# Kernel tuning notes

Hardware: AMD Instinct MI355X
Metric: run time of the kernel (lower is better)

Reference implementation:

```python
import jax, jax.numpy as jnp
import numpy as np

B, T, LEAF, A = 128, 50, 4880, 64
INTERNAL = 728
ATTN = 128   # attn_dim_size (GRU input)
RNN = 128    # rnn_dim_size
G = 128      # g_dim_size (== RNN, required by broadcast in forward)
NC = 283     # num_class
VERY_NEG = -1e30


def setup_inputs() -> dict:
    key = jax.random.key(0)
    ks = jax.random.split(key, 16)
    s = 0.05
    inputs_x = jax.random.uniform(ks[0], (B, T, LEAF), jnp.float32)
    inputs_f = jax.random.randint(ks[1], (B, T, A), 0, INTERNAL + 1)  # 0 = padding
    mask_seqs = jnp.ones((B, T), jnp.float32)
    dag_emb = jax.random.normal(ks[2], (LEAF, ATTN), jnp.float32) * s
    embed_a = jax.random.normal(ks[3], (INTERNAL + 1, G), jnp.float32) * s
    embed_a = embed_a.at[0].set(0.0)  # padding row
    # 2-layer GRU params (torch layout: [3H, in], gates r,z,n)
    Wih0 = jax.random.normal(ks[4], (3 * RNN, ATTN), jnp.float32) * s
    Whh0 = jax.random.normal(ks[5], (3 * RNN, RNN), jnp.float32) * s
    bih0 = jax.random.normal(ks[6], (3 * RNN,), jnp.float32) * s
    bhh0 = jax.random.normal(ks[7], (3 * RNN,), jnp.float32) * s
    Wih1 = jax.random.normal(ks[8], (3 * RNN, RNN), jnp.float32) * s
    Whh1 = jax.random.normal(ks[9], (3 * RNN, RNN), jnp.float32) * s
    bih1 = jax.random.normal(ks[10], (3 * RNN,), jnp.float32) * s
    bhh1 = jax.random.normal(ks[11], (3 * RNN,), jnp.float32) * s
    fc_w = jax.random.normal(ks[12], (NC, 2 * RNN), jnp.float32) * s
    fc_b = jax.random.normal(ks[13], (NC,), jnp.float32) * s
    return dict(inputs_x=inputs_x, inputs_f=inputs_f, mask_seqs=mask_seqs,
                dag_emb=dag_emb, embed_a=embed_a,
                Wih0=Wih0, Whh0=Whh0, bih0=bih0, bhh0=bhh0,
                Wih1=Wih1, Whh1=Whh1, bih1=bih1, bhh1=bhh1,
                fc_w=fc_w, fc_b=fc_b)


def _gru_layer(x, Wih, Whh, bih, bhh):
    # x: [B, T, I] -> out [B, T, H]; h0 = zeros
    H = Whh.shape[1]
    xW = jnp.einsum('bti,gi->btg', x, Wih) + bih  # [B,T,3H], precompute input gates
    h0 = jnp.zeros((x.shape[0], H), x.dtype)

    def step(h, xw_t):  # xw_t: [B,3H]
        gh = h @ Whh.T + bhh
        xr, xz, xn = jnp.split(xw_t, 3, axis=-1)
        hr, hz, hn = jnp.split(gh, 3, axis=-1)
        r = jax.nn.sigmoid(xr + hr)
        z = jax.nn.sigmoid(xz + hz)
        n = jnp.tanh(xn + r * hn)
        h_new = (1.0 - z) * n + z * h
        return h_new, h_new

    _, ys = jax.lax.scan(step, h0, jnp.swapaxes(xW, 0, 1))  # scan over T
    return jnp.swapaxes(ys, 0, 1)


def reference(inputs_x, inputs_f, mask_seqs, dag_emb, embed_a,
              Wih0, Whh0, bih0, bhh0, Wih1, Whh1, bih1, bhh1, fc_w, fc_b):
    # x = tanh(inputs_x @ dag_emb): [B,T,ATTN]
    x = jnp.tanh(jnp.einsum('btl,la->bta', inputs_x, dag_emb))
    # 2-layer GRU (no dropout at inference)
    h1 = _gru_layer(x, Wih0, Whh0, bih0, bhh0)
    out = _gru_layer(h1, Wih1, Whh1, bih1, bhh1)  # [B,T,RNN]
    # gather ancestor embeddings: [B,T,A,G]
    l = embed_a[inputs_f]
    # masked dot-product attention over ancestors
    hl = jnp.einsum('bth,btah->bta', out, l)
    mask_ans = inputs_f > 0
    hl = hl + jnp.where(mask_ans, 0.0, VERY_NEG)
    weights = jax.nn.softmax(hl, axis=-1)  # [B,T,A]
    k = jnp.einsum('bta,btah->bth', weights, l)
    s = jnp.concatenate([out, k], axis=-1)  # [B,T,2*RNN]
    output = jax.nn.sigmoid(s @ fc_w.T + fc_b)
    return output * mask_seqs[:, :, None]
```

## Files before the change

kernel.cpp:

```cpp
#include <hip/hip_runtime.h>
#include <math.h>

#define B_DIM 128
#define T_DIM 50
#define LEAF  4880
#define A_DIM 64
#define ATTN  128
#define RNN   128
#define NC    283
#define M_TOT (B_DIM*T_DIM)
#define KSPLIT 10
#define NCH 153
#define WT_PLANE (NCH*512*8)

using short8 = __attribute__((ext_vector_type(8))) short;
using short4v = __attribute__((ext_vector_type(4))) short;
using f32x4  = __attribute__((ext_vector_type(4))) float;

__device__ __forceinline__ float sigmoidf_(float x) {
  return 1.0f / (1.0f + __expf(-x));
}
__device__ __forceinline__ float tanhf_fast(float x) {
  x = fminf(fmaxf(x, -15.f), 15.f);
  float e = __expf(2.f * x);
  return (e - 1.f) * __builtin_amdgcn_rcpf(e + 1.f);
}

__device__ __forceinline__ unsigned short f32_to_bf16_rne(float f) {
  unsigned int u = __float_as_uint(f);
  unsigned int r = u + 0x7FFFu + ((u >> 16) & 1u);
  return (unsigned short)(r >> 16);
}
__device__ __forceinline__ float bf16_bits_to_f32(unsigned short b) {
  return __uint_as_float(((unsigned int)b) << 16);
}

__global__ __launch_bounds__(256) void k_prep(
    const float* __restrict__ Wd,
    const float* __restrict__ Wih0, const float* __restrict__ Wih1,
    const float* __restrict__ fcw,
    unsigned short* __restrict__ Wt,
    unsigned short* __restrict__ Bt0, unsigned short* __restrict__ Bt1,
    unsigned short* __restrict__ Bt2) {
  const int bx = blockIdx.x;
  const int tid = threadIdx.x;
  if (bx < 306) {
    const int u = bx * 256 + tid;
    const int c = u >> 9, rem = u & 511;
    const int nt = rem >> 6, lane = rem & 63;
    const int n = nt * 16 + (lane & 15);
    const int kb = c * 32 + ((lane >> 4) << 3);
    short8 h8, l8;
    #pragma unroll
    for (int j = 0; j < 8; ++j) {
      int k = kb + j;
      float v = (k < LEAF) ? Wd[(size_t)k * 128 + n] : 0.0f;
      unsigned short hb = f32_to_bf16_rne(v);
      unsigned short lb = f32_to_bf16_rne(v - bf16_bits_to_f32(hb));
      h8[j] = (short)hb;
      l8[j] = (short)lb;
    }
    *(short8*)&Wt[(size_t)u * 8] = h8;
    *(short8*)&Wt[(size_t)WT_PLANE + (size_t)u * 8] = l8;
  } else {
    const float* src; unsigned short* dst; int N, K, s0;
    if (bx < 330)      { src = Wih0; dst = Bt0; N = 384; K = 128; s0 = (bx - 306) * 256; }
    else if (bx < 354) { src = Wih1; dst = Bt1; N = 384; K = 128; s0 = (bx - 330) * 256; }
    else               { src = fcw;  dst = Bt2; N = NC;  K = 256; s0 = (bx - 354) * 256; }
    const int s = s0 + tid;
    const int PL = (K / 32) * 24 * 512;
    const int kc = s / (24 * 64);
    const int r  = s % (24 * 64);
    const int nt = r >> 6, lane = r & 63;
    const int n  = nt * 16 + (lane & 15);
    const int kb = kc * 32 + ((lane >> 4) << 3);
    short8 h8, l8;
    #pragma unroll
    for (int j = 0; j < 8; ++j) {
      float v = (n < N) ? src[(size_t)n * K + kb + j] : 0.0f;
      unsigned short hb = f32_to_bf16_rne(v);
      unsigned short lb = f32_to_bf16_rne(v - bf16_bits_to_f32(hb));
      h8[j] = (short)hb;
      l8[j] = (short)lb;
    }
    *(short8*)&dst[(size_t)s * 8] = h8;
    *(short8*)&dst[(size_t)PL + (size_t)s * 8] = l8;
  }
}

__global__ __launch_bounds__(512, 8) void k_gemm_mfma(
    const float* __restrict__ Ax, const unsigned short* __restrict__ Wt,
    float* __restrict__ P) {
  __shared__ __align__(16) unsigned short As[2][4096];
  const int tid  = threadIdx.x;
  const int lane = tid & 63;
  const int w    = tid >> 6;
  const int M0   = blockIdx.x * 64;
  const int s    = blockIdx.y;
  const int c0   = (s * NCH) / KSPLIT;
  const int c1   = ((s + 1) * NCH) / KSPLIT;

  const int am = tid >> 3;
  const int kq = tid & 7;
  const float* pA = Ax + (size_t)(M0 + am) * LEAF;
  const int a_idx = (am >> 4) * 512 + ((am & 15) + 16 * (kq >> 1)) * 8 + (kq & 1) * 4;

  f32x4 acc[4];
  #pragma unroll
  for (int i = 0; i < 4; ++i) {
    #pragma unroll
    for (int q = 0; q < 4; ++q) acc[i][q] = 0.0f;
  }

  float4 rA_a, rA_b;
  short8 bh_a, bl_a, bh_b, bl_b;

  auto issueB = [&](int c, short8& bh, short8& bl) {
    const size_t o = ((size_t)c * 512 + w * 64 + lane) * 8;
    bh = *(const short8*)&Wt[o];
    bl = *(const short8*)&Wt[(size_t)WT_PLANE + o];
  };
  auto issueA = [&](int c, float4& ra) {
    int kk = c * 32 + kq * 4;
    kk = min(kk, LEAF - 4);
    ra = *(const float4*)(pA + kk);
  };
  auto storeA = [&](int p, float4 ra) {
    float v[4] = {ra.x, ra.y, ra.z, ra.w};
    short4v h4, l4;
    #pragma unroll
    for (int j = 0; j < 4; ++j) {
      unsigned short hb = f32_to_bf16_rne(v[j]);
      unsigned short lb = f32_to_bf16_rne(v[j] - bf16_bits_to_f32(hb));
      h4[j] = (short)hb;
      l4[j] = (short)lb;
    }
    *(short4v*)&As[p][a_idx] = h4;
    *(short4v*)&As[p][2048 + a_idx] = l4;
  };
  auto compute = [&](int p, const short8& bh, const short8& bl) {
    #pragma unroll
    for (int m = 0; m < 4; ++m) {
      short8 a_hi = *(const short8*)&As[p][m * 512 + lane * 8];
      short8 a_lo = *(const short8*)&As[p][2048 + m * 512 + lane * 8];
      acc[m] = __builtin_amdgcn_mfma_f32_16x16x32_bf16(a_hi, bl, acc[m], 0, 0, 0);
      acc[m] = __builtin_amdgcn_mfma_f32_16x16x32_bf16(a_lo, bh, acc[m], 0, 0, 0);
      acc[m] = __builtin_amdgcn_mfma_f32_16x16x32_bf16(a_hi, bh, acc[m], 0, 0, 0);
    }
  };

  {
    float4 ta;
    issueA(c0, ta);
    asm volatile("s_waitcnt vmcnt(0)" ::: "memory");
    storeA(0, ta);
    issueB(c0, bh_a, bl_a);
    asm volatile("" ::: "memory");
    if (c0 + 1 < c1) issueA(c0 + 1, rA_a);
    asm volatile("s_waitcnt lgkmcnt(0)" ::: "memory");
    __builtin_amdgcn_s_barrier();
    asm volatile("" ::: "memory");
  }

#define GEMM_ITER(BHc, BLc, BHn, BLn, RAc, RAn)                               \
  {                                                                           \
    const int p = (c - c0) & 1;                                               \
    const bool has1 = (c + 1 < c1), has2 = (c + 2 < c1);                      \
    if (has1) { issueB(c + 1, BHn, BLn); asm volatile("" ::: "memory"); }     \
    if (has2) { issueA(c + 2, RAn);      asm volatile("" ::: "memory"); }     \
    if (has1) {                                                               \
      if (has2) { asm volatile("s_waitcnt vmcnt(3)" ::: "memory"); }          \
      else      { asm volatile("s_waitcnt vmcnt(2)" ::: "memory"); }          \
    } else      { asm volatile("s_waitcnt vmcnt(0)" ::: "memory"); }          \
    compute(p, BHc, BLc);                                                     \
    if (has1) storeA(p ^ 1, RAc);                                             \
    asm volatile("s_waitcnt lgkmcnt(0)" ::: "memory");                        \
    __builtin_amdgcn_s_barrier();                                             \
    asm volatile("" ::: "memory");                                            \
    ++c;                                                                      \
  }

  int c = c0;
  while (c < c1) {
    GEMM_ITER(bh_a, bl_a, bh_b, bl_b, rA_a, rA_b);
    if (c < c1) GEMM_ITER(bh_b, bl_b, bh_a, bl_a, rA_b, rA_a);
  }
#undef GEMM_ITER

  float* outp = P + (size_t)s * ((size_t)M_TOT * 128);
  const int col0 = w * 16 + (lane & 15);
  #pragma unroll
  for (int m = 0; m < 4; ++m) {
    const int rbase = M0 + m * 16 + ((lane >> 4) << 2);
    #pragma unroll
    for (int r = 0; r < 4; ++r)
      outp[(size_t)(rbase + r) * 128 + col0] = acc[m][r];
  }
}

__global__ __launch_bounds__(256) void k_reduce_tanh(
    float* __restrict__ P, float* __restrict__ X) {
  const size_t i = ((size_t)blockIdx.x * 256 + threadIdx.x) * 4;
  float4 a = *(const float4*)&P[i];
  #pragma unroll
  for (int s = 1; s < KSPLIT; ++s) {
    float4 b = *(const float4*)&P[(size_t)s * (M_TOT * 128) + i];
    a.x += b.x; a.y += b.y; a.z += b.z; a.w += b.w;
  }
  a.x = tanhf(a.x); a.y = tanhf(a.y); a.z = tanhf(a.z); a.w = tanhf(a.w);
  *(float4*)&X[i] = a;
}

template<int KC, int ACT>
__global__ __launch_bounds__(512) void k_bn_mfma(
    const float* __restrict__ A, const unsigned short* __restrict__ Bt,
    const float* __restrict__ bias, const float* __restrict__ maskv,
    float* __restrict__ C, int N, int ldc) {
  constexpr int K  = KC * 32;
  constexpr int PL = KC * 24 * 512;
  __shared__ __align__(16) unsigned short As2[2][KC * 512];
  const int tid  = threadIdx.x;
  const int lane = tid & 63;
  const int w    = tid >> 6;
  const int mrow = blockIdx.x * 16;
  const int nt   = blockIdx.y * 8 + w;

  short8 bh[KC], bl[KC];
  #pragma unroll
  for (int kc = 0; kc < KC; ++kc) {
    const size_t o = ((size_t)(kc * 24 + nt) * 64 + lane) * 8;
    bh[kc] = *(const short8*)&Bt[o];
    bl[kc] = *(const short8*)&Bt[(size_t)PL + o];
  }

  const int am = tid >> 5;
  const int q0 = tid & 31;
  constexpr int NQ = K / 128;
  float4 av[NQ];
  #pragma unroll
  for (int i = 0; i < NQ; ++i)
    av[i] = *(const float4*)&A[(size_t)(mrow + am) * K + (q0 + 32 * i) * 4];
  #pragma unroll
  for (int i = 0; i < NQ; ++i) {
    const int q = q0 + 32 * i;
    const int base = (am + 16 * (q >> 1)) * 8 + (q & 1) * 4;
    float v[4] = {av[i].x, av[i].y, av[i].z, av[i].w};
    short4v h4, l4;
    #pragma unroll
    for (int j = 0; j < 4; ++j) {
      unsigned short hb = f32_to_bf16_rne(v[j]);
      unsigned short lb = f32_to_bf16_rne(v[j] - bf16_bits_to_f32(hb));
      h4[j] = (short)hb;
      l4[j] = (short)lb;
    }
    *(short4v*)&As2[0][base] = h4;
    *(short4v*)&As2[1][base] = l4;
  }
  __syncthreads();

  f32x4 acc;
  #pragma unroll
  for (int q = 0; q < 4; ++q) acc[q] = 0.0f;
  #pragma unroll
  for (int kc = 0; kc < KC; ++kc) {
    const int slot = (lane & 15) + 64 * kc + 16 * (lane >> 4);
    short8 a_hi = *(const short8*)&As2[0][slot * 8];
    short8 a_lo = *(const short8*)&As2[1][slot * 8];
    acc = __builtin_amdgcn_mfma_f32_16x16x32_bf16(a_hi, bl[kc], acc, 0, 0, 0);
    acc = __builtin_amdgcn_mfma_f32_16x16x32_bf16(a_lo, bh[kc], acc, 0, 0, 0);
    acc = __builtin_amdgcn_mfma_f32_16x16x32_bf16(a_hi, bh[kc], acc, 0, 0, 0);
  }

  const int col = nt * 16 + (lane & 15);
  if (col < N) {
    const float bv = bias[col];
    #pragma unroll
    for (int r = 0; r < 4; ++r) {
      const int m = mrow + ((lane >> 4) << 2) + r;
      float v = acc[r] + bv;
      if (ACT) v = sigmoidf_(v) * maskv[m];
      C[(size_t)m * ldc + col] = v;
    }
  }
}

__global__ __launch_bounds__(512) void k_gru(
    const float* __restrict__ xW, const float* __restrict__ Whh,
    const float* __restrict__ bhh, float* __restrict__ Hout) {
  const int b = blockIdx.x;
  const int tid = threadIdx.x;
  const int j  = tid >> 2;
  const int qf = tid & 3;
  __shared__ __align__(16) float hs[2][128];

  float4 wr[8], wz[8], wn[8];
  {
    const float* pr = Whh + (size_t)j * 128 + qf * 32;
    const float* pz = Whh + (size_t)(j + 128) * 128 + qf * 32;
    const float* pn = Whh + (size_t)(j + 256) * 128 + qf * 32;
    #pragma unroll
    for (int k = 0; k < 8; ++k) {
      const int c = (k + qf * 2) & 7;
      wr[k] = *(const float4*)(pr + c * 4);
      wz[k] = *(const float4*)(pz + c * 4);
      wn[k] = *(const float4*)(pn + c * 4);
    }
  }
  const float br = bhh[j], bz = bhh[j + 128], bn_ = bhh[j + 256];

  if (tid < 128) hs[0][tid] = 0.0f;
  const float* xwb = xW + (size_t)b * 50 * 384;
  float xr = 0.f, xz = 0.f, xn = 0.f;
  if (qf == 0) { xr = xwb[j]; xz = xwb[128 + j]; xn = xwb[256 + j]; }
  __syncthreads();

  int cur = 0;
  for (int t = 0; t < 50; ++t) {
    float nxr = 0.f, nxz = 0.f, nxn = 0.f;
    if (qf == 0 && t + 1 < 50) {
      const float* xwn = xwb + (size_t)(t + 1) * 384;
      nxr = xwn[j]; nxz = xwn[128 + j]; nxn = xwn[256 + j];
    }

    float ar = 0.f, az = 0.f, an = 0.f;
    #pragma unroll
    for (int k = 0; k < 8; ++k) {
      const int c = (k + qf * 2) & 7;
      float4 hv = *(const float4*)&hs[cur][qf * 32 + c * 4];
      ar += wr[k].x * hv.x + wr[k].y * hv.y + wr[k].z * hv.z + wr[k].w * hv.w;
      az += wz[k].x * hv.x + wz[k].y * hv.y + wz[k].z * hv.z + wz[k].w * hv.w;
      an += wn[k].x * hv.x + wn[k].y * hv.y + wn[k].z * hv.z + wn[k].w * hv.w;
    }
    ar += __shfl_xor(ar, 1); ar += __shfl_xor(ar, 2);
    az += __shfl_xor(az, 1); az += __shfl_xor(az, 2);
    an += __shfl_xor(an, 1); an += __shfl_xor(an, 2);

    if (qf == 0) {
      float r = sigmoidf_(xr + ar + br);
      float z = sigmoidf_(xz + az + bz);
      float nn = tanhf_fast(xn + r * (an + bn_));
      float h = (1.f - z) * nn + z * hs[cur][j];
      hs[cur ^ 1][j] = h;
      Hout[(size_t)(b * 50 + t) * 128 + j] = h;
    }
    __syncthreads();
    cur ^= 1;
    xr = nxr; xz = nxz; xn = nxn;
  }
}

__global__ __launch_bounds__(128) void k_attn(
    const float* __restrict__ H2, const int* __restrict__ F,
    const float* __restrict__ emb, float* __restrict__ S) {
  const int m = blockIdx.x;
  const int tid = threadIdx.x;
  __shared__ __align__(16) float outs[128];
  __shared__ __align__(16) float Ls[64][132];
  __shared__ float hls[64];
  __shared__ float wts[64];
  __shared__ int fs[64];

  outs[tid] = H2[(size_t)m * 128 + tid];
  if (tid < 64) fs[tid] = F[(size_t)m * 64 + tid];
  __syncthreads();

  #pragma unroll
  for (int i = 0; i < 16; ++i) {
    int idx = tid + i * 128;
    int a = idx >> 5, c4 = idx & 31;
    float4 v = *(const float4*)&emb[(size_t)fs[a] * 128 + c4 * 4];
    *(float4*)&Ls[a][c4 * 4] = v;
  }
  __syncthreads();

  {
    const int a = tid >> 1, hf = tid & 1;
    float sum = 0.f;
    #pragma unroll
    for (int j = 0; j < 16; ++j) {
      float4 lv = *(const float4*)&Ls[a][hf * 64 + j * 4];
      float4 ov = *(const float4*)&outs[hf * 64 + j * 4];
      sum += lv.x * ov.x + lv.y * ov.y + lv.z * ov.z + lv.w * ov.w;
    }
    float other = __shfl_xor(sum, 1);
    sum += other;
    if (hf == 0) hls[a] = sum + (fs[a] > 0 ? 0.0f : -1e30f);
  }
  __syncthreads();

  if (tid < 64) {
    float v = hls[tid];
    float mx = v;
    #pragma unroll
    for (int o = 32; o; o >>= 1) mx = fmaxf(mx, __shfl_xor(mx, o));
    float e = __expf(v - mx);
    float sm = e;
    #pragma unroll
    for (int o = 32; o; o >>= 1) sm += __shfl_xor(sm, o);
    wts[tid] = e / sm;
  }
  __syncthreads();

  float kv = 0.f;
  #pragma unroll 8
  for (int a2 = 0; a2 < 64; ++a2) kv += wts[a2] * Ls[a2][tid];

  S[(size_t)m * 256 + tid] = outs[tid];
  S[(size_t)m * 256 + 128 + tid] = kv;
}

extern "C" void kernel_launch(void* const* d_in, const int* in_sizes, int n_in,
                              void* d_out, int out_size, void* d_ws, size_t ws_size,
                              hipStream_t stream) {
  const float* inputs_x  = (const float*)d_in[0];
  const int*   inputs_f  = (const int*)d_in[1];
  const float* mask_seqs = (const float*)d_in[2];
  const float* dag_emb   = (const float*)d_in[3];
  const float* embed_a   = (const float*)d_in[4];
  const float* Wih0 = (const float*)d_in[5];
  const float* Whh0 = (const float*)d_in[6];
  const float* bih0 = (const float*)d_in[7];
  const float* bhh0 = (const float*)d_in[8];
  const float* Wih1 = (const float*)d_in[9];
  const float* Whh1 = (const float*)d_in[10];
  const float* bih1 = (const float*)d_in[11];
  const float* bhh1 = (const float*)d_in[12];
  const float* fc_w = (const float*)d_in[13];
  const float* fc_b = (const float*)d_in[14];
  float* out = (float*)d_out;

  float* ws = (float*)d_ws;
  float* P  = ws;
  float* X  = P;
  float* S  = P + 819200;
  float* xW = ws + KSPLIT * 819200;
  float* H1 = xW + 2457600;
  float* H2 = H1 + 819200;
  unsigned short* Wt  = (unsigned short*)H1;
  unsigned short* Bt0 = (unsigned short*)(H2 + 819200);
  unsigned short* Bt1 = Bt0 + 2 * 49152;
  unsigned short* Bt2 = Bt1 + 2 * 49152;

  k_prep<<<402, 256, 0, stream>>>(dag_emb, Wih0, Wih1, fc_w, Wt, Bt0, Bt1, Bt2);
  k_gemm_mfma<<<dim3(100, KSPLIT), 512, 0, stream>>>(inputs_x, Wt, P);
  k_reduce_tanh<<<800, 256, 0, stream>>>(P, X);
  k_bn_mfma<4, 0><<<dim3(400, 3), 512, 0, stream>>>(X, Bt0, bih0, nullptr, xW, 384, 384);
  k_gru<<<128, 512, 0, stream>>>(xW, Whh0, bhh0, H1);
  k_bn_mfma<4, 0><<<dim3(400, 3), 512, 0, stream>>>(H1, Bt1, bih1, nullptr, xW, 384, 384);
  k_gru<<<128, 512, 0, stream>>>(xW, Whh1, bhh1, H2);
  k_attn<<<6400, 128, 0, stream>>>(H2, inputs_f, embed_a, S);
  k_bn_mfma<8, 1><<<dim3(400, 3), 512, 0, stream>>>(S, Bt2, fc_b, mask_seqs, out, NC, NC);
}
```

Before: 369.3 us.

## Fuse split-K reduce+tanh into GRU input GEMM and drop concat buffer

Removes the separate split-K reduction/tanh kernel by having the first input-projection GEMM sum the KSPLIT partials and apply tanh while loading its A tile. The final FC GEMM now reads H2 and the attention context from two separate buffers instead of a concatenated S buffer, and the attention kernel reads embedding rows directly from global memory instead of staging them in LDS. The grid is also transposed so that consecutive blocks share the same M rows. In exchange, each first-GEMM block re-reduces the partials for its rows once per N-block (3x), and the attention kernel issues more global loads that depend on L1/L2 hits for the gathered rows.

```diff
diff --git a/kernel.cpp b/kernel.cpp
--- a/kernel.cpp
+++ b/kernel.cpp
@@ -198,22 +198,10 @@
   }
 }
 
-__global__ __launch_bounds__(256) void k_reduce_tanh(
-    float* __restrict__ P, float* __restrict__ X) {
-  const size_t i = ((size_t)blockIdx.x * 256 + threadIdx.x) * 4;
-  float4 a = *(const float4*)&P[i];
-  #pragma unroll
-  for (int s = 1; s < KSPLIT; ++s) {
-    float4 b = *(const float4*)&P[(size_t)s * (M_TOT * 128) + i];
-    a.x += b.x; a.y += b.y; a.z += b.z; a.w += b.w;
-  }
-  a.x = tanhf(a.x); a.y = tanhf(a.y); a.z = tanhf(a.z); a.w = tanhf(a.w);
-  *(float4*)&X[i] = a;
-}
-
-template<int KC, int ACT>
+template<int KC, int ACT, int MODE>
 __global__ __launch_bounds__(512) void k_bn_mfma(
-    const float* __restrict__ A, const unsigned short* __restrict__ Bt,
+    const float* __restrict__ A0, const float* __restrict__ A1,
+    const unsigned short* __restrict__ Bt,
     const float* __restrict__ bias, const float* __restrict__ maskv,
     float* __restrict__ C, int N, int ldc) {
   constexpr int K  = KC * 32;
@@ -222,8 +210,8 @@
   const int tid  = threadIdx.x;
   const int lane = tid & 63;
   const int w    = tid >> 6;
-  const int mrow = blockIdx.x * 16;
-  const int nt   = blockIdx.y * 8 + w;
+  const int nt   = blockIdx.x * 8 + w;
+  const int mrow = blockIdx.y * 16;
 
   short8 bh[KC], bl[KC];
   #pragma unroll
@@ -237,9 +225,24 @@
   const int q0 = tid & 31;
   constexpr int NQ = K / 128;
   float4 av[NQ];
-  #pragma unroll
-  for (int i = 0; i < NQ; ++i)
-    av[i] = *(const float4*)&A[(size_t)(mrow + am) * K + (q0 + 32 * i) * 4];
+  if (MODE == 1) {
+    const float* p = A0 + (size_t)(mrow + am) * 128 + q0 * 4;
+    float4 a = *(const float4*)p;
+    #pragma unroll
+    for (int s = 1; s < KSPLIT; ++s) {
+      float4 b = *(const float4*)(p + (size_t)s * (M_TOT * 128));
+      a.x += b.x; a.y += b.y; a.z += b.z; a.w += b.w;
+    }
+    av[0].x = tanhf(a.x); av[0].y = tanhf(a.y);
+    av[0].z = tanhf(a.z); av[0].w = tanhf(a.w);
+  } else if (MODE == 2) {
+    av[0] = *(const float4*)&A0[(size_t)(mrow + am) * 128 + q0 * 4];
+    av[1] = *(const float4*)&A1[(size_t)(mrow + am) * 128 + q0 * 4];
+  } else {
+    #pragma unroll
+    for (int i = 0; i < NQ; ++i)
+      av[i] = *(const float4*)&A0[(size_t)(mrow + am) * K + (q0 + 32 * i) * 4];
+  }
   #pragma unroll
   for (int i = 0; i < NQ; ++i) {
     const int q = q0 + 32 * i;
@@ -351,11 +354,10 @@
 
 __global__ __launch_bounds__(128) void k_attn(
     const float* __restrict__ H2, const int* __restrict__ F,
-    const float* __restrict__ emb, float* __restrict__ S) {
+    const float* __restrict__ emb, float* __restrict__ Katt) {
   const int m = blockIdx.x;
   const int tid = threadIdx.x;
   __shared__ __align__(16) float outs[128];
-  __shared__ __align__(16) float Ls[64][132];
   __shared__ float hls[64];
   __shared__ float wts[64];
   __shared__ int fs[64];
@@ -364,21 +366,13 @@
   if (tid < 64) fs[tid] = F[(size_t)m * 64 + tid];
   __syncthreads();
 
-  #pragma unroll
-  for (int i = 0; i < 16; ++i) {
-    int idx = tid + i * 128;
-    int a = idx >> 5, c4 = idx & 31;
-    float4 v = *(const float4*)&emb[(size_t)fs[a] * 128 + c4 * 4];
-    *(float4*)&Ls[a][c4 * 4] = v;
-  }
-  __syncthreads();
-
   {
     const int a = tid >> 1, hf = tid & 1;
+    const float* er = emb + (size_t)fs[a] * 128 + hf * 64;
     float sum = 0.f;
     #pragma unroll
     for (int j = 0; j < 16; ++j) {
-      float4 lv = *(const float4*)&Ls[a][hf * 64 + j * 4];
+      float4 lv = *(const float4*)&er[j * 4];
       float4 ov = *(const float4*)&outs[hf * 64 + j * 4];
       sum += lv.x * ov.x + lv.y * ov.y + lv.z * ov.z + lv.w * ov.w;
     }
@@ -403,10 +397,10 @@
 
   float kv = 0.f;
   #pragma unroll 8
-  for (int a2 = 0; a2 < 64; ++a2) kv += wts[a2] * Ls[a2][tid];
-
-  S[(size_t)m * 256 + tid] = outs[tid];
-  S[(size_t)m * 256 + 128 + tid] = kv;
+  for (int a2 = 0; a2 < 64; ++a2)
+    kv += wts[a2] * emb[(size_t)fs[a2] * 128 + tid];
+
+  Katt[(size_t)m * 128 + tid] = kv;
 }
 
 extern "C" void kernel_launch(void* const* d_in, const int* in_sizes, int n_in,
@@ -430,9 +424,8 @@
   float* out = (float*)d_out;
 
   float* ws = (float*)d_ws;
-  float* P  = ws;
-  float* X  = P;
-  float* S  = P + 819200;
+  float* P    = ws;
+  float* Katt = P + 819200;
   float* xW = ws + KSPLIT * 819200;
   float* H1 = xW + 2457600;
   float* H2 = H1 + 819200;
@@ -443,11 +436,10 @@
 
   k_prep<<<402, 256, 0, stream>>>(dag_emb, Wih0, Wih1, fc_w, Wt, Bt0, Bt1, Bt2);
   k_gemm_mfma<<<dim3(100, KSPLIT), 512, 0, stream>>>(inputs_x, Wt, P);
-  k_reduce_tanh<<<800, 256, 0, stream>>>(P, X);
-  k_bn_mfma<4, 0><<<dim3(400, 3), 512, 0, stream>>>(X, Bt0, bih0, nullptr, xW, 384, 384);
+  k_bn_mfma<4, 0, 1><<<dim3(3, 400), 512, 0, stream>>>(P, nullptr, Bt0, bih0, nullptr, xW, 384, 384);
   k_gru<<<128, 512, 0, stream>>>(xW, Whh0, bhh0, H1);
-  k_bn_mfma<4, 0><<<dim3(400, 3), 512, 0, stream>>>(H1, Bt1, bih1, nullptr, xW, 384, 384);
+  k_bn_mfma<4, 0, 0><<<dim3(3, 400), 512, 0, stream>>>(H1, nullptr, Bt1, bih1, nullptr, xW, 384, 384);
   k_gru<<<128, 512, 0, stream>>>(xW, Whh1, bhh1, H2);
-  k_attn<<<6400, 128, 0, stream>>>(H2, inputs_f, embed_a, S);
-  k_bn_mfma<8, 1><<<dim3(400, 3), 512, 0, stream>>>(S, Bt2, fc_b, mask_seqs, out, NC, NC);
-}
+  k_attn<<<6400, 128, 0, stream>>>(H2, inputs_f, embed_a, Katt);
+  k_bn_mfma<8, 1, 2><<<dim3(3, 400), 512, 0, stream>>>(H2, Katt, Bt2, fc_b, mask_seqs, out, NC, NC);
+}
```

Result: slower. 383.0 us (+3.7%).
